# Kernel tuning notes

Hardware: AMD Instinct MI355X
Metric: run time of the kernel (lower is better)

The kernel has to match this reference:

```python
import jax, jax.numpy as jnp
import numpy as np

P = 8           # patch size
IMG = 256       # image size
C_IN = 64       # indim
HEADS = 32
DIM = P * P * C_IN          # 4096
SCALE = (DIM / HEADS) ** -0.5  # uses dim/heads = 128, as in the torch code
EPS = 1e-5


def unfold(x):
    # x: [B, C, H, W] -> [B, N, C*P*P]  (torch Unfold channel order: c, ki, kj)
    B, C, H, W = x.shape
    x = x.reshape(B, C, H // P, P, W // P, P)
    x = x.transpose(0, 1, 3, 5, 2, 4)           # [B, C, P, P, H/P, W/P]
    x = x.reshape(B, C * P * P, (H // P) * (W // P))
    return x.transpose(0, 2, 1)                  # b n c


def fold(x):
    # x: [B, C*P*P, N] -> [B, C, IMG, IMG]  (non-overlapping: exact inverse)
    B, Cpp, N = x.shape
    C = Cpp // (P * P)
    hp = IMG // P
    x = x.reshape(B, C, P, P, hp, hp)
    x = x.transpose(0, 1, 4, 2, 5, 3)            # [B, C, H/P, P, W/P, P]
    return x.reshape(B, C, IMG, IMG)


def layernorm(x, g, b):
    mu = jnp.mean(x, axis=-1, keepdims=True)
    var = jnp.mean(jnp.square(x - mu), axis=-1, keepdims=True)
    return (x - mu) * jax.lax.rsqrt(var + EPS) * g + b


def heads_split(x):
    # b n (g c) -> b g n c
    B, N, GC = x.shape
    return x.reshape(B, N, HEADS, GC // HEADS).transpose(0, 2, 1, 3)


def setup_inputs() -> dict:
    key = jax.random.key(0)
    ks = jax.random.split(key, 16)
    d = DIM
    def lin(k, din, dout):
        return jax.random.normal(k, (din, dout), jnp.float32) * (din ** -0.5)
    return {
        "pan": jax.random.normal(ks[0], (2, C_IN, IMG, IMG), jnp.float32),
        "ms": jax.random.normal(ks[1], (2, C_IN, IMG, IMG), jnp.float32),
        "g_q": jnp.ones((2 * d,), jnp.float32), "b_q": jnp.zeros((2 * d,), jnp.float32),
        "g_kp": jnp.ones((d,), jnp.float32), "b_kp": jnp.zeros((d,), jnp.float32),
        "g_vp": jnp.ones((d,), jnp.float32), "b_vp": jnp.zeros((d,), jnp.float32),
        "g_km": jnp.ones((d,), jnp.float32), "b_km": jnp.zeros((d,), jnp.float32),
        "g_vm": jnp.ones((d,), jnp.float32), "b_vm": jnp.zeros((d,), jnp.float32),
        "w_q": lin(ks[2], 2 * d, d // 4),
        "w_kp": lin(ks[3], d, d // 4),
        "w_vp": lin(ks[4], d, d),
        "w_km": lin(ks[5], d, d // 4),
        "w_vm": lin(ks[6], d, d),
    }


def _forward(pan, ms, g_q, b_q, g_kp, b_kp, g_vp, b_vp, g_km, b_km, g_vm, b_vm,
             w_q, w_kp, w_vp, w_km, w_vm):
    u_q = unfold(jnp.concatenate([pan, ms], axis=1))      # [B, N, 2*DIM]
    u_p = unfold(pan)                                     # [B, N, DIM]
    u_m = unfold(ms)                                      # [B, N, DIM]

    q = heads_split(layernorm(u_q, g_q, b_q) @ w_q)       # [B, G, N, 32]
    k_pan = heads_split(layernorm(u_p, g_kp, b_kp) @ w_kp)
    v_pan = heads_split(layernorm(u_p, g_vp, b_vp) @ w_vp)  # [B, G, N, 128]
    k_ms = heads_split(layernorm(u_m, g_km, b_km) @ w_km)
    v_ms = heads_split(layernorm(u_m, g_vm, b_vm) @ w_vm)

    def attend(k, v):
        logits = jnp.einsum('bgnc,bgmc->bgnm', q, k) * SCALE
        a = jax.nn.softmax(logits, axis=-1)
        o = jnp.einsum('bgnm,bgmc->bgnc', a, v)           # [B, G, N, 128]
        B, G, N, c = o.shape
        o = o.transpose(0, 2, 1, 3).reshape(B, N, G * c)  # b n (g c)
        return fold(o.transpose(0, 2, 1))                 # [B, C_IN, IMG, IMG]

    out_pan = attend(k_pan, v_pan) + pan
    out_ms = attend(k_ms, v_ms) + ms
    return jnp.concatenate([out_pan, out_ms], axis=1)


def reference(pan, ms, g_q, b_q, g_kp, b_kp, g_vp, b_vp, g_km, b_km, g_vm, b_vm,
              w_q, w_kp, w_vp, w_km, w_vm):
    return _forward(pan, ms, g_q, b_q, g_kp, b_kp, g_vp, b_vp, g_km, b_km,
                    g_vm, b_vm, w_q, w_kp, w_vp, w_km, w_vm)
```

## Files before the change

### kernel.cpp

```cpp
#include <hip/hip_runtime.h>
#include <hip/hip_bf16.h>

typedef __attribute__((ext_vector_type(8))) __bf16 bf16x8;
typedef __attribute__((ext_vector_type(8))) short s16x8;
typedef __attribute__((ext_vector_type(4))) float f32x4;

#define DEVI __device__ __forceinline__

DEVI f32x4 mfma16(bf16x8 a, bf16x8 b, f32x4 c) {
  return __builtin_amdgcn_mfma_f32_16x16x32_bf16((s16x8)a, (s16x8)b, c, 0, 0, 0);
}

constexpr float SCALE = 0.08838834764831845f;

constexpr size_t MB = 1024ull * 1024ull;
constexpr size_t OFF_WQT  = 0;
constexpr size_t OFF_WKPT = 16 * MB;
constexpr size_t OFF_WKMT = 24 * MB;
constexpr size_t OFF_LNQ  = 32 * MB;
constexpr size_t OFF_WVPT = 0;
constexpr size_t OFF_WVMT = 32 * MB;
constexpr size_t OFF_LNP  = 64 * MB;
constexpr size_t OFF_LNM  = 80 * MB;
constexpr size_t OFF_Q    = 96 * MB;
constexpr size_t OFF_KP   = 100 * MB;
constexpr size_t OFF_KM   = 104 * MB;
constexpr size_t OFF_VPT  = 108 * MB;
constexpr size_t OFF_VMT  = 124 * MB;
constexpr size_t OFF_BQ   = 140 * MB;
constexpr size_t OFF_BKP  = OFF_BQ  + 1024 * 4;
constexpr size_t OFF_BKM  = OFF_BKP + 1024 * 4;
constexpr size_t OFF_BVP  = OFF_BKM + 1024 * 4;
constexpr size_t OFF_BVM  = OFF_BVP + 4096 * 4;
constexpr int    N_BIAS_F = 3 * 1024 + 2 * 4096;

DEVI void async16(void* lds, const void* g) {
  __builtin_amdgcn_global_load_lds(
      (const __attribute__((address_space(1))) void*)g,
      (__attribute__((address_space(3))) void*)lds, 16, 0, 0);
}

__global__ void zero_kernel(float* p, int n) {
  int i = blockIdx.x * 256 + threadIdx.x;
  if (i < n) p[i] = 0.f;
}

__global__ __launch_bounds__(256) void wconv_kernel(
    const float* __restrict__ W, const float* __restrict__ gam,
    const float* __restrict__ bet, __bf16* __restrict__ wT,
    float* __restrict__ biasOut, int K, int N) {
  __shared__ float tile[64][65];
  const int n0 = blockIdx.x * 64, k0 = blockIdx.y * 64;
  const int t = threadIdx.x;
  const int nl = t & 63, kb = t >> 6;
  float pb = 0.f;
#pragma unroll
  for (int i = 0; i < 16; ++i) {
    const int kl = kb * 16 + i;
    const int k = k0 + kl;
    const float w = W[(long)k * N + n0 + nl];
    tile[kl][nl] = w * gam[k];
    pb += bet[k] * w;
  }
  atomicAdd(biasOut + n0 + nl, pb);
  __syncthreads();
  const int klw = t & 63;
#pragma unroll
  for (int i = 0; i < 16; ++i) {
    const int nloc = kb * 16 + i;
    wT[(long)(n0 + nloc) * K + k0 + klw] = (__bf16)tile[klw][nloc];
  }
}

__global__ __launch_bounds__(256) void ln_kernel(
    const float* __restrict__ pan, const float* __restrict__ ms,
    __bf16* __restrict__ lnq, __bf16* __restrict__ lnp, __bf16* __restrict__ lnm) {
  const int bid = blockIdx.x;
  const int b = bid >> 10, n = bid & 1023;
  const int ph = n >> 5, pw = n & 31;
  const int t = threadIdx.x;
  const int c = t >> 2, kp2 = t & 3;

  const long base = ((long)(b * 64 + c) << 16) + (long)(ph * 8) * 256 + pw * 8;
  float rp[16], rm[16];
#pragma unroll
  for (int kk = 0; kk < 2; ++kk) {
    const int ki = kp2 * 2 + kk;
    const f32x4* p0 = (const f32x4*)(pan + base + ki * 256);
    const f32x4* m0 = (const f32x4*)(ms + base + ki * 256);
    f32x4 pa = p0[0], pb = p0[1], ma = m0[0], mb = m0[1];
#pragma unroll
    for (int j = 0; j < 4; ++j) {
      rp[kk * 8 + j] = pa[j];
      rp[kk * 8 + 4 + j] = pb[j];
      rm[kk * 8 + j] = ma[j];
      rm[kk * 8 + 4 + j] = mb[j];
    }
  }
  float sp = 0, sp2 = 0, smm = 0, sm2 = 0;
#pragma unroll
  for (int j = 0; j < 16; ++j) {
    sp += rp[j]; sp2 += rp[j] * rp[j];
    smm += rm[j]; sm2 += rm[j] * rm[j];
  }
#pragma unroll
  for (int msk = 1; msk < 64; msk <<= 1) {
    sp += __shfl_xor(sp, msk);
    sp2 += __shfl_xor(sp2, msk);
    smm += __shfl_xor(smm, msk);
    sm2 += __shfl_xor(sm2, msk);
  }
  __shared__ float red[4][4];
  const int wid = t >> 6;
  if ((t & 63) == 0) { red[wid][0] = sp; red[wid][1] = sp2; red[wid][2] = smm; red[wid][3] = sm2; }
  __syncthreads();
  sp = red[0][0] + red[1][0] + red[2][0] + red[3][0];
  sp2 = red[0][1] + red[1][1] + red[2][1] + red[3][1];
  smm = red[0][2] + red[1][2] + red[2][2] + red[3][2];
  sm2 = red[0][3] + red[1][3] + red[2][3] + red[3][3];

  const float mu_p = sp * (1.f / 4096.f);
  const float rs_p = rsqrtf(sp2 * (1.f / 4096.f) - mu_p * mu_p + 1e-5f);
  const float mu_m = smm * (1.f / 4096.f);
  const float rs_m = rsqrtf(sm2 * (1.f / 4096.f) - mu_m * mu_m + 1e-5f);
  const float mu_q = (sp + smm) * (1.f / 8192.f);
  const float rs_q = rsqrtf((sp2 + sm2) * (1.f / 8192.f) - mu_q * mu_q + 1e-5f);

  const long row = bid;
  const int f0 = t * 16;
  bf16x8 v0, v1;
#pragma unroll
  for (int j = 0; j < 8; ++j) { v0[j] = (__bf16)((rp[j] - mu_p) * rs_p); v1[j] = (__bf16)((rp[8 + j] - mu_p) * rs_p); }
  *(bf16x8*)(lnp + row * 4096 + f0) = v0;
  *(bf16x8*)(lnp + row * 4096 + f0 + 8) = v1;
#pragma unroll
  for (int j = 0; j < 8; ++j) { v0[j] = (__bf16)((rm[j] - mu_m) * rs_m); v1[j] = (__bf16)((rm[8 + j] - mu_m) * rs_m); }
  *(bf16x8*)(lnm + row * 4096 + f0) = v0;
  *(bf16x8*)(lnm + row * 4096 + f0 + 8) = v1;
#pragma unroll
  for (int j = 0; j < 8; ++j) { v0[j] = (__bf16)((rp[j] - mu_q) * rs_q); v1[j] = (__bf16)((rp[8 + j] - mu_q) * rs_q); }
  *(bf16x8*)(lnq + row * 8192 + f0) = v0;
  *(bf16x8*)(lnq + row * 8192 + f0 + 8) = v1;
#pragma unroll
  for (int j = 0; j < 8; ++j) { v0[j] = (__bf16)((rm[j] - mu_q) * rs_q); v1[j] = (__bf16)((rm[8 + j] - mu_q) * rs_q); }
  *(bf16x8*)(lnq + row * 8192 + 4096 + f0) = v0;
  *(bf16x8*)(lnq + row * 8192 + 4096 + f0 + 8) = v1;
}

struct G3 {
  const __bf16 *X0, *X1, *X2, *Y0, *Y1, *Y2;
  __bf16 *O0, *O1, *O2;
  const float *bX0, *bX1, *bX2, *bY0, *bY1, *bY2;
  int K0, K1, K2, M2;
};

__global__ __launch_bounds__(256, 2) void gemm_batch(G3 g) {
  const int z = blockIdx.z;
  const __bf16* X = z == 0 ? g.X0 : (z == 1 ? g.X1 : g.X2);
  const __bf16* Y = z == 0 ? g.Y0 : (z == 1 ? g.Y1 : g.Y2);
  __bf16* out = z == 0 ? g.O0 : (z == 1 ? g.O1 : g.O2);
  const float* biasX = z == 0 ? g.bX0 : (z == 1 ? g.bX1 : g.bX2);
  const float* biasY = z == 0 ? g.bY0 : (z == 1 ? g.bY1 : g.bY2);
  const int K = z == 0 ? g.K0 : (z == 1 ? g.K1 : g.K2);
  const int M2 = g.M2;

  __shared__ __bf16 xt[128 * 32];
  __shared__ __bf16 yt[128 * 32];
  const int t = threadIdx.x;
  const int lane = t & 63, wid = t >> 6;
  const int wr = wid >> 1, wc = wid & 1;
  const int l15 = lane & 15, l4 = lane >> 4;
  const long x0 = (long)blockIdx.x * 128;
  const long y0 = (long)blockIdx.y * 128;

  f32x4 acc[4][4] = {};

  for (int kk = 0; kk < K; kk += 32) {
    __syncthreads();
#pragma unroll
    for (int i = 0; i < 2; ++i) {
      const int chunk = i * 256 + t;
      const int r = chunk >> 2, q = chunk & 3;
      async16((char*)xt + (i * 256 + wid * 64) * 16, X + (x0 + r) * K + kk + q * 8);
      async16((char*)yt + (i * 256 + wid * 64) * 16, Y + (y0 + r) * K + kk + q * 8);
    }
    __syncthreads();
    bf16x8 a[4], bb[4];
#pragma unroll
    for (int mi = 0; mi < 4; ++mi)
      a[mi] = *(const bf16x8*)(xt + (wr * 64 + mi * 16 + l15) * 32 + l4 * 8);
#pragma unroll
    for (int ni = 0; ni < 4; ++ni)
      bb[ni] = *(const bf16x8*)(yt + (wc * 64 + ni * 16 + l15) * 32 + l4 * 8);
#pragma unroll
    for (int mi = 0; mi < 4; ++mi)
#pragma unroll
      for (int ni = 0; ni < 4; ++ni)
        acc[mi][ni] = mfma16(a[mi], bb[ni], acc[mi][ni]);
  }

#pragma unroll
  for (int mi = 0; mi < 4; ++mi) {
#pragma unroll
    for (int r = 0; r < 4; ++r) {
      const long row = x0 + wr * 64 + mi * 16 + l4 * 4 + r;
      const float bx = biasX ? biasX[row] : 0.f;
#pragma unroll
      for (int ni = 0; ni < 4; ++ni) {
        const long col = y0 + wc * 64 + ni * 16 + l15;
        const float by = biasY ? biasY[col] : 0.f;
        out[row * M2 + col] = (__bf16)(acc[mi][ni][r] + bx + by);
      }
    }
  }
}

__global__ __launch_bounds__(256, 2) void attn_kernel(
    const __bf16* __restrict__ Qm, const __bf16* __restrict__ Kpm,
    const __bf16* __restrict__ Kmm, const __bf16* __restrict__ VpT,
    const __bf16* __restrict__ VmT, const float* __restrict__ pan,
    const float* __restrict__ ms, float* __restrict__ out) {
  __shared__ __bf16 ktile[128 * 32];
  __shared__ __bf16 vtile[128 * 128];
  __shared__ __bf16 ptile[4][32 * 128];

  const int bid = blockIdx.x;
  const int qt = bid & 7, g = (bid >> 3) & 31, tt = (bid >> 8) & 1, b = bid >> 9;
  const __bf16* Kmat = tt ? Kmm : Kpm;
  const __bf16* VT = tt ? VmT : VpT;
  const float* res = tt ? ms : pan;

  const int t = threadIdx.x, lane = t & 63, wid = t >> 6;
  const int l15 = lane & 15, l4 = lane >> 4;

  bf16x8 qf[2];
#pragma unroll
  for (int mi = 0; mi < 2; ++mi) {
    const long row = (long)b * 1024 + qt * 128 + wid * 32 + mi * 16 + l15;
    qf[mi] = *(const bf16x8*)(Qm + row * 1024 + g * 32 + l4 * 8);
  }

  f32x4 acc[2][8] = {};
  float mrun[2][4], lrun[2][4];
#pragma unroll
  for (int mi = 0; mi < 2; ++mi)
#pragma unroll
    for (int r = 0; r < 4; ++r) { mrun[mi][r] = -1e30f; lrun[mi][r] = 0.f; }

  for (int kt = 0; kt < 8; ++kt) {
    __syncthreads();
#pragma unroll
    for (int i = 0; i < 2; ++i) {
      const int chunk = i * 256 + t;
      const int key = chunk >> 2, slot = chunk & 3;
      const int q = slot ^ ((key >> 1) & 3);
      async16((char*)ktile + (i * 256 + wid * 64) * 16,
              Kmat + (long)(b * 1024 + kt * 128 + key) * 1024 + g * 32 + q * 8);
    }
#pragma unroll
    for (int i = 0; i < 8; ++i) {
      const int chunk = i * 256 + t;
      const int d = chunk >> 4, slot = chunk & 15;
      const int c16 = slot ^ (d & 15);
      async16((char*)vtile + (i * 256 + wid * 64) * 16,
              VT + (long)(g * 128 + d) * 2048 + b * 1024 + kt * 128 + c16 * 8);
    }
    __syncthreads();

    f32x4 s[2][8];
#pragma unroll
    for (int ni = 0; ni < 8; ++ni) {
      const int key = ni * 16 + l15;
      const int slot = l4 ^ ((key >> 1) & 3);
      const bf16x8 kf = *(const bf16x8*)(ktile + key * 32 + slot * 8);
      f32x4 zz = {0.f, 0.f, 0.f, 0.f};
      s[0][ni] = mfma16(qf[0], kf, zz);
      s[1][ni] = mfma16(qf[1], kf, zz);
    }

#pragma unroll
    for (int mi = 0; mi < 2; ++mi) {
#pragma unroll
      for (int r = 0; r < 4; ++r) {
        float tmax = -1e30f;
#pragma unroll
        for (int ni = 0; ni < 8; ++ni) tmax = fmaxf(tmax, s[mi][ni][r]);
        tmax *= SCALE;
#pragma unroll
        for (int msk = 1; msk < 16; msk <<= 1) tmax = fmaxf(tmax, __shfl_xor(tmax, msk));
        const float mnew = fmaxf(mrun[mi][r], tmax);
        const float alpha = __expf(mrun[mi][r] - mnew);
        mrun[mi][r] = mnew;
        float tsum = 0.f;
#pragma unroll
        for (int ni = 0; ni < 8; ++ni) {
          const float p = __expf(s[mi][ni][r] * SCALE - mnew);
          s[mi][ni][r] = p;
          tsum += p;
        }
#pragma unroll
        for (int msk = 1; msk < 16; msk <<= 1) tsum += __shfl_xor(tsum, msk);
        lrun[mi][r] = lrun[mi][r] * alpha + tsum;
#pragma unroll
        for (int ni = 0; ni < 8; ++ni) acc[mi][ni][r] *= alpha;
      }
    }

#pragma unroll
    for (int mi = 0; mi < 2; ++mi)
#pragma unroll
      for (int ni = 0; ni < 8; ++ni)
#pragma unroll
        for (int r = 0; r < 4; ++r) {
          const int q = mi * 16 + l4 * 4 + r;
          const int key = ni * 16 + l15;
          const int off = q * 256 + (((key >> 3) ^ (q & 15)) * 16) + (key & 7) * 2;
          *(__bf16*)((char*)ptile[wid] + off) = (__bf16)s[mi][ni][r];
        }
    __syncthreads();

#pragma unroll
    for (int ks = 0; ks < 4; ++ks) {
      bf16x8 pa[2];
#pragma unroll
      for (int mi = 0; mi < 2; ++mi) {
        const int q = mi * 16 + l15;
        const int slot = (ks * 4 + l4) ^ (q & 15);
        pa[mi] = *(const bf16x8*)((char*)ptile[wid] + q * 256 + slot * 16);
      }
#pragma unroll
      for (int ni = 0; ni < 8; ++ni) {
        const int d = ni * 16 + l15;
        const int slot = (ks * 4 + l4) ^ (d & 15);
        const bf16x8 vf = *(const bf16x8*)((char*)vtile + d * 256 + slot * 16);
        acc[0][ni] = mfma16(pa[0], vf, acc[0][ni]);
        acc[1][ni] = mfma16(pa[1], vf, acc[1][ni]);
      }
    }
  }

#pragma unroll
  for (int mi = 0; mi < 2; ++mi) {
#pragma unroll
    for (int r = 0; r < 4; ++r) {
      const float inv = 1.f / lrun[mi][r];
      const int n = qt * 128 + wid * 32 + mi * 16 + l4 * 4 + r;
      const int ph = n >> 5, pw = n & 31;
#pragma unroll
      for (int ni = 0; ni < 8; ++ni) {
        const int d = ni * 16 + l15;
        const int ch = 2 * g + (d >> 6);
        const int pix = (ph * 8 + ((d >> 3) & 7)) * 256 + pw * 8 + (d & 7);
        const long ridx = (long)(b * 64 + ch) * 65536 + pix;
        const long oidx = (long)(b * 128 + tt * 64 + ch) * 65536 + pix;
        out[oidx] = acc[mi][ni][r] * inv + res[ridx];
      }
    }
  }
}

extern "C" void kernel_launch(void* const* d_in, const int* in_sizes, int n_in,
                              void* d_out, int out_size, void* d_ws, size_t ws_size,
                              hipStream_t stream) {
  const float* pan = (const float*)d_in[0];
  const float* ms = (const float*)d_in[1];
  const float* g_q = (const float*)d_in[2];
  const float* b_q = (const float*)d_in[3];
  const float* g_kp = (const float*)d_in[4];
  const float* b_kp = (const float*)d_in[5];
  const float* g_vp = (const float*)d_in[6];
  const float* b_vp = (const float*)d_in[7];
  const float* g_km = (const float*)d_in[8];
  const float* b_km = (const float*)d_in[9];
  const float* g_vm = (const float*)d_in[10];
  const float* b_vm = (const float*)d_in[11];
  const float* w_q = (const float*)d_in[12];
  const float* w_kp = (const float*)d_in[13];
  const float* w_vp = (const float*)d_in[14];
  const float* w_km = (const float*)d_in[15];
  const float* w_vm = (const float*)d_in[16];

  char* ws = (char*)d_ws;
  __bf16* wqT = (__bf16*)(ws + OFF_WQT);
  __bf16* wkpT = (__bf16*)(ws + OFF_WKPT);
  __bf16* wkmT = (__bf16*)(ws + OFF_WKMT);
  __bf16* lnq = (__bf16*)(ws + OFF_LNQ);
  __bf16* wvpT = (__bf16*)(ws + OFF_WVPT);
  __bf16* wvmT = (__bf16*)(ws + OFF_WVMT);
  __bf16* lnp = (__bf16*)(ws + OFF_LNP);
  __bf16* lnm = (__bf16*)(ws + OFF_LNM);
  __bf16* Qm = (__bf16*)(ws + OFF_Q);
  __bf16* Kpm = (__bf16*)(ws + OFF_KP);
  __bf16* Kmm = (__bf16*)(ws + OFF_KM);
  __bf16* VpT = (__bf16*)(ws + OFF_VPT);
  __bf16* VmT = (__bf16*)(ws + OFF_VMT);
  float* bq = (float*)(ws + OFF_BQ);
  float* bkp = (float*)(ws + OFF_BKP);
  float* bkm = (float*)(ws + OFF_BKM);
  float* bvp = (float*)(ws + OFF_BVP);
  float* bvm = (float*)(ws + OFF_BVM);

  const dim3 blk(256);

  zero_kernel<<<(N_BIAS_F + 255) / 256, blk, 0, stream>>>(bq, N_BIAS_F);

  wconv_kernel<<<dim3(16, 128), blk, 0, stream>>>(w_q, g_q, b_q, wqT, bq, 8192, 1024);
  wconv_kernel<<<dim3(16, 64), blk, 0, stream>>>(w_kp, g_kp, b_kp, wkpT, bkp, 4096, 1024);
  wconv_kernel<<<dim3(16, 64), blk, 0, stream>>>(w_km, g_km, b_km, wkmT, bkm, 4096, 1024);

  ln_kernel<<<2048, blk, 0, stream>>>(pan, ms, lnq, lnp, lnm);

  {
    G3 g;
    g.X0 = lnq; g.X1 = lnp; g.X2 = lnm;
    g.Y0 = wqT; g.Y1 = wkpT; g.Y2 = wkmT;
    g.O0 = Qm; g.O1 = Kpm; g.O2 = Kmm;
    g.bX0 = nullptr; g.bX1 = nullptr; g.bX2 = nullptr;
    g.bY0 = bq; g.bY1 = bkp; g.bY2 = bkm;
    g.K0 = 8192; g.K1 = 4096; g.K2 = 4096; g.M2 = 1024;
    gemm_batch<<<dim3(16, 8, 3), blk, 0, stream>>>(g);
  }

  wconv_kernel<<<dim3(64, 64), blk, 0, stream>>>(w_vp, g_vp, b_vp, wvpT, bvp, 4096, 4096);
  wconv_kernel<<<dim3(64, 64), blk, 0, stream>>>(w_vm, g_vm, b_vm, wvmT, bvm, 4096, 4096);

  {
    G3 g;
    g.X0 = wvpT; g.X1 = wvmT; g.X2 = wvmT;
    g.Y0 = lnp; g.Y1 = lnm; g.Y2 = lnm;
    g.O0 = VpT; g.O1 = VmT; g.O2 = VmT;
    g.bX0 = bvp; g.bX1 = bvm; g.bX2 = bvm;
    g.bY0 = nullptr; g.bY1 = nullptr; g.bY2 = nullptr;
    g.K0 = 4096; g.K1 = 4096; g.K2 = 4096; g.M2 = 2048;
    gemm_batch<<<dim3(32, 16, 2), blk, 0, stream>>>(g);
  }

  attn_kernel<<<1024, blk, 0, stream>>>(Qm, Kpm, Kmm, VpT, VmT, pan, ms, (float*)d_out);
}
```

Baseline: 826.4 us.

## Halve attention key tiles for higher occupancy and swizzle GEMM block order

The attention kernel now processes keys in 64-key tiles instead of 128, which cuts shared memory per block. It raises the launch-bounds occupancy target from 2 to 4 blocks per CU and reorders block IDs so each query tile is the outer index over batch, type and head. The batched GEMM remaps its 2D block index with a stride-8 interleave to change L2 and XCD locality of tile scheduling. The trade-off is twice as many softmax rescale steps and barriers per block, plus tighter register limits that may cause spills.

```diff
diff --git a/kernel.cpp b/kernel.cpp
--- a/kernel.cpp
+++ b/kernel.cpp
@@ -164,14 +164,19 @@
   const int K = z == 0 ? g.K0 : (z == 1 ? g.K1 : g.K2);
   const int M2 = g.M2;
 
+  int lh = blockIdx.x + gridDim.x * blockIdx.y;
+  const int per = (gridDim.x * gridDim.y) >> 3;
+  lh = (lh & 7) * per + (lh >> 3);
+  const int bx = lh % gridDim.x, by = lh / gridDim.x;
+
   __shared__ __bf16 xt[128 * 32];
   __shared__ __bf16 yt[128 * 32];
   const int t = threadIdx.x;
   const int lane = t & 63, wid = t >> 6;
   const int wr = wid >> 1, wc = wid & 1;
   const int l15 = lane & 15, l4 = lane >> 4;
-  const long x0 = (long)blockIdx.x * 128;
-  const long y0 = (long)blockIdx.y * 128;
+  const long x0 = (long)bx * 128;
+  const long y0 = (long)by * 128;
 
   f32x4 acc[4][4] = {};
 
@@ -204,28 +209,29 @@
 #pragma unroll
     for (int r = 0; r < 4; ++r) {
       const long row = x0 + wr * 64 + mi * 16 + l4 * 4 + r;
-      const float bx = biasX ? biasX[row] : 0.f;
+      const float bx_ = biasX ? biasX[row] : 0.f;
 #pragma unroll
       for (int ni = 0; ni < 4; ++ni) {
         const long col = y0 + wc * 64 + ni * 16 + l15;
-        const float by = biasY ? biasY[col] : 0.f;
-        out[row * M2 + col] = (__bf16)(acc[mi][ni][r] + bx + by);
+        const float by_ = biasY ? biasY[col] : 0.f;
+        out[row * M2 + col] = (__bf16)(acc[mi][ni][r] + bx_ + by_);
       }
     }
   }
 }
 
-__global__ __launch_bounds__(256, 2) void attn_kernel(
+__global__ __launch_bounds__(256, 4) void attn_kernel(
     const __bf16* __restrict__ Qm, const __bf16* __restrict__ Kpm,
     const __bf16* __restrict__ Kmm, const __bf16* __restrict__ VpT,
     const __bf16* __restrict__ VmT, const float* __restrict__ pan,
     const float* __restrict__ ms, float* __restrict__ out) {
-  __shared__ __bf16 ktile[128 * 32];
-  __shared__ __bf16 vtile[128 * 128];
-  __shared__ __bf16 ptile[4][32 * 128];
+  __shared__ __bf16 ktile[64 * 32];
+  __shared__ __bf16 vtile[128 * 64];
+  __shared__ __bf16 ptile[4][32 * 64];
 
   const int bid = blockIdx.x;
-  const int qt = bid & 7, g = (bid >> 3) & 31, tt = (bid >> 8) & 1, b = bid >> 9;
+  const int qt = bid >> 7, gid = bid & 127;
+  const int b = gid >> 6, tt = (gid >> 5) & 1, g = gid & 31;
   const __bf16* Kmat = tt ? Kmm : Kpm;
   const __bf16* VT = tt ? VmT : VpT;
   const float* res = tt ? ms : pan;
@@ -247,29 +253,27 @@
 #pragma unroll
     for (int r = 0; r < 4; ++r) { mrun[mi][r] = -1e30f; lrun[mi][r] = 0.f; }
 
-  for (int kt = 0; kt < 8; ++kt) {
+  for (int kt = 0; kt < 16; ++kt) {
     __syncthreads();
-#pragma unroll
-    for (int i = 0; i < 2; ++i) {
+    {
+      const int key = t >> 2, slot = t & 3;
+      const int q = slot ^ ((key >> 1) & 3);
+      async16((char*)ktile + t * 16,
+              Kmat + (long)(b * 1024 + kt * 64 + key) * 1024 + g * 32 + q * 8);
+    }
+#pragma unroll
+    for (int i = 0; i < 4; ++i) {
       const int chunk = i * 256 + t;
-      const int key = chunk >> 2, slot = chunk & 3;
-      const int q = slot ^ ((key >> 1) & 3);
-      async16((char*)ktile + (i * 256 + wid * 64) * 16,
-              Kmat + (long)(b * 1024 + kt * 128 + key) * 1024 + g * 32 + q * 8);
-    }
-#pragma unroll
-    for (int i = 0; i < 8; ++i) {
-      const int chunk = i * 256 + t;
-      const int d = chunk >> 4, slot = chunk & 15;
-      const int c16 = slot ^ (d & 15);
-      async16((char*)vtile + (i * 256 + wid * 64) * 16,
-              VT + (long)(g * 128 + d) * 2048 + b * 1024 + kt * 128 + c16 * 8);
+      const int d = chunk >> 3, slot = chunk & 7;
+      const int c8 = slot ^ (d & 7);
+      async16((char*)vtile + chunk * 16,
+              VT + (long)(g * 128 + d) * 2048 + b * 1024 + kt * 64 + c8 * 8);
     }
     __syncthreads();
 
-    f32x4 s[2][8];
-#pragma unroll
-    for (int ni = 0; ni < 8; ++ni) {
+    f32x4 s[2][4];
+#pragma unroll
+    for (int ni = 0; ni < 4; ++ni) {
       const int key = ni * 16 + l15;
       const int slot = l4 ^ ((key >> 1) & 3);
       const bf16x8 kf = *(const bf16x8*)(ktile + key * 32 + slot * 8);
@@ -284,7 +288,7 @@
       for (int r = 0; r < 4; ++r) {
         float tmax = -1e30f;
 #pragma unroll
-        for (int ni = 0; ni < 8; ++ni) tmax = fmaxf(tmax, s[mi][ni][r]);
+        for (int ni = 0; ni < 4; ++ni) tmax = fmaxf(tmax, s[mi][ni][r]);
         tmax *= SCALE;
 #pragma unroll
         for (int msk = 1; msk < 16; msk <<= 1) tmax = fmaxf(tmax, __shfl_xor(tmax, msk));
@@ -293,7 +297,7 @@
         mrun[mi][r] = mnew;
         float tsum = 0.f;
 #pragma unroll
-        for (int ni = 0; ni < 8; ++ni) {
+        for (int ni = 0; ni < 4; ++ni) {
           const float p = __expf(s[mi][ni][r] * SCALE - mnew);
           s[mi][ni][r] = p;
           tsum += p;
@@ -302,37 +306,39 @@
         for (int msk = 1; msk < 16; msk <<= 1) tsum += __shfl_xor(tsum, msk);
         lrun[mi][r] = lrun[mi][r] * alpha + tsum;
 #pragma unroll
-        for (int ni = 0; ni < 8; ++ni) acc[mi][ni][r] *= alpha;
+        for (int ni = 0; ni < 4; ++ni) acc[mi][ni][r] *= alpha;
+#pragma unroll
+        for (int ni = 4; ni < 8; ++ni) acc[mi][ni][r] *= alpha;
       }
     }
 
 #pragma unroll
     for (int mi = 0; mi < 2; ++mi)
 #pragma unroll
-      for (int ni = 0; ni < 8; ++ni)
+      for (int ni = 0; ni < 4; ++ni)
 #pragma unroll
         for (int r = 0; r < 4; ++r) {
           const int q = mi * 16 + l4 * 4 + r;
           const int key = ni * 16 + l15;
-          const int off = q * 256 + (((key >> 3) ^ (q & 15)) * 16) + (key & 7) * 2;
+          const int off = q * 128 + (((key >> 3) ^ (q & 7)) * 16) + (key & 7) * 2;
           *(__bf16*)((char*)ptile[wid] + off) = (__bf16)s[mi][ni][r];
         }
     __syncthreads();
 
 #pragma unroll
-    for (int ks = 0; ks < 4; ++ks) {
+    for (int ks = 0; ks < 2; ++ks) {
       bf16x8 pa[2];
 #pragma unroll
       for (int mi = 0; mi < 2; ++mi) {
         const int q = mi * 16 + l15;
-        const int slot = (ks * 4 + l4) ^ (q & 15);
-        pa[mi] = *(const bf16x8*)((char*)ptile[wid] + q * 256 + slot * 16);
+        const int slot = (ks * 4 + l4) ^ (q & 7);
+        pa[mi] = *(const bf16x8*)((char*)ptile[wid] + q * 128 + slot * 16);
       }
 #pragma unroll
       for (int ni = 0; ni < 8; ++ni) {
         const int d = ni * 16 + l15;
-        const int slot = (ks * 4 + l4) ^ (d & 15);
-        const bf16x8 vf = *(const bf16x8*)((char*)vtile + d * 256 + slot * 16);
+        const int slot = (ks * 4 + l4) ^ (d & 7);
+        const bf16x8 vf = *(const bf16x8*)((char*)vtile + d * 128 + slot * 16);
         acc[0][ni] = mfma16(pa[0], vf, acc[0][ni]);
         acc[1][ni] = mfma16(pa[1], vf, acc[1][ni]);
       }
```

After: 1.021 ms. 1.24x slower.

## Keep softmax probabilities in registers via transposed MFMA and vectorize epilogue stores

Applied to the files above, without the earlier changes.

The attention kernel computes S^T by swapping MFMA operands and permuting the key rows as they load into LDS, so the probability tile already has the register layout needed as the B operand of the PV MFMA. This removes the per-warp LDS round trip for P and the extra __syncthreads. Softmax statistics become one value per row per lane, reduced across lanes with two shuffles. LDS use falls, so launch bounds go to 3 blocks per CU. The epilogue stages each output tile through LDS and writes it with 16-byte vectorized residual loads and stores. The GEMM also swizzles its block indices for better cache locality. Risks include register pressure at the higher occupancy and subtle layout errors in the key permutation.

```diff
diff --git a/kernel.cpp b/kernel.cpp
--- a/kernel.cpp
+++ b/kernel.cpp
@@ -2,6 +2,7 @@
 #include <hip/hip_bf16.h>
 
 typedef __attribute__((ext_vector_type(8))) __bf16 bf16x8;
+typedef __attribute__((ext_vector_type(4))) __bf16 bf16x4;
 typedef __attribute__((ext_vector_type(8))) short s16x8;
 typedef __attribute__((ext_vector_type(4))) float f32x4;
 
@@ -164,14 +165,19 @@
   const int K = z == 0 ? g.K0 : (z == 1 ? g.K1 : g.K2);
   const int M2 = g.M2;
 
+  int lh = blockIdx.x + gridDim.x * blockIdx.y;
+  const int per = (gridDim.x * gridDim.y) >> 3;
+  lh = (lh & 7) * per + (lh >> 3);
+  const int bx = lh % gridDim.x, by = lh / gridDim.x;
+
   __shared__ __bf16 xt[128 * 32];
   __shared__ __bf16 yt[128 * 32];
   const int t = threadIdx.x;
   const int lane = t & 63, wid = t >> 6;
   const int wr = wid >> 1, wc = wid & 1;
   const int l15 = lane & 15, l4 = lane >> 4;
-  const long x0 = (long)blockIdx.x * 128;
-  const long y0 = (long)blockIdx.y * 128;
+  const long x0 = (long)bx * 128;
+  const long y0 = (long)by * 128;
 
   f32x4 acc[4][4] = {};
 
@@ -204,25 +210,25 @@
 #pragma unroll
     for (int r = 0; r < 4; ++r) {
       const long row = x0 + wr * 64 + mi * 16 + l4 * 4 + r;
-      const float bx = biasX ? biasX[row] : 0.f;
+      const float bx_ = biasX ? biasX[row] : 0.f;
 #pragma unroll
       for (int ni = 0; ni < 4; ++ni) {
         const long col = y0 + wc * 64 + ni * 16 + l15;
-        const float by = biasY ? biasY[col] : 0.f;
-        out[row * M2 + col] = (__bf16)(acc[mi][ni][r] + bx + by);
+        const float by_ = biasY ? biasY[col] : 0.f;
+        out[row * M2 + col] = (__bf16)(acc[mi][ni][r] + bx_ + by_);
       }
     }
   }
 }
 
-__global__ __launch_bounds__(256, 2) void attn_kernel(
+__global__ __launch_bounds__(256, 3) void attn_kernel(
     const __bf16* __restrict__ Qm, const __bf16* __restrict__ Kpm,
     const __bf16* __restrict__ Kmm, const __bf16* __restrict__ VpT,
     const __bf16* __restrict__ VmT, const float* __restrict__ pan,
     const float* __restrict__ ms, float* __restrict__ out) {
-  __shared__ __bf16 ktile[128 * 32];
-  __shared__ __bf16 vtile[128 * 128];
-  __shared__ __bf16 ptile[4][32 * 128];
+  __shared__ char smem[40960];
+  __bf16* ktile = (__bf16*)smem;
+  __bf16* vtile = (__bf16*)(smem + 8192);
 
   const int bid = blockIdx.x;
   const int qt = bid & 7, g = (bid >> 3) & 31, tt = (bid >> 8) & 1, b = bid >> 9;
@@ -241,21 +247,18 @@
   }
 
   f32x4 acc[2][8] = {};
-  float mrun[2][4], lrun[2][4];
-#pragma unroll
-  for (int mi = 0; mi < 2; ++mi)
-#pragma unroll
-    for (int r = 0; r < 4; ++r) { mrun[mi][r] = -1e30f; lrun[mi][r] = 0.f; }
+  float mrun[2] = {-1e30f, -1e30f}, lrun[2] = {0.f, 0.f};
 
   for (int kt = 0; kt < 8; ++kt) {
     __syncthreads();
 #pragma unroll
     for (int i = 0; i < 2; ++i) {
       const int chunk = i * 256 + t;
-      const int key = chunk >> 2, slot = chunk & 3;
-      const int q = slot ^ ((key >> 1) & 3);
+      const int rho = chunk >> 2, slot = chunk & 3;
+      const int cq = slot ^ ((rho >> 1) & 3);
+      const int keyg = 32 * (rho >> 5) + 8 * ((rho >> 2) & 3) + 4 * ((rho >> 4) & 1) + (rho & 3);
       async16((char*)ktile + (i * 256 + wid * 64) * 16,
-              Kmat + (long)(b * 1024 + kt * 128 + key) * 1024 + g * 32 + q * 8);
+              Kmat + (long)(b * 1024 + kt * 128 + keyg) * 1024 + g * 32 + cq * 8);
     }
 #pragma unroll
     for (int i = 0; i < 8; ++i) {
@@ -267,95 +270,95 @@
     }
     __syncthreads();
 
-    f32x4 s[2][8];
-#pragma unroll
-    for (int ni = 0; ni < 8; ++ni) {
-      const int key = ni * 16 + l15;
-      const int slot = l4 ^ ((key >> 1) & 3);
-      const bf16x8 kf = *(const bf16x8*)(ktile + key * 32 + slot * 8);
-      f32x4 zz = {0.f, 0.f, 0.f, 0.f};
-      s[0][ni] = mfma16(qf[0], kf, zz);
-      s[1][ni] = mfma16(qf[1], kf, zz);
-    }
-
+    bf16x4 pk[2][8];
 #pragma unroll
     for (int mi = 0; mi < 2; ++mi) {
-#pragma unroll
-      for (int r = 0; r < 4; ++r) {
-        float tmax = -1e30f;
-#pragma unroll
-        for (int ni = 0; ni < 8; ++ni) tmax = fmaxf(tmax, s[mi][ni][r]);
-        tmax *= SCALE;
-#pragma unroll
-        for (int msk = 1; msk < 16; msk <<= 1) tmax = fmaxf(tmax, __shfl_xor(tmax, msk));
-        const float mnew = fmaxf(mrun[mi][r], tmax);
-        const float alpha = __expf(mrun[mi][r] - mnew);
-        mrun[mi][r] = mnew;
-        float tsum = 0.f;
-#pragma unroll
-        for (int ni = 0; ni < 8; ++ni) {
-          const float p = __expf(s[mi][ni][r] * SCALE - mnew);
-          s[mi][ni][r] = p;
+      f32x4 s[8];
+#pragma unroll
+      for (int ni = 0; ni < 8; ++ni) {
+        const int pos = ni * 16 + l15;
+        const int slot = l4 ^ ((pos >> 1) & 3);
+        const bf16x8 kf = *(const bf16x8*)(ktile + pos * 32 + slot * 8);
+        f32x4 zz = {0.f, 0.f, 0.f, 0.f};
+        s[ni] = mfma16(kf, qf[mi], zz);
+      }
+      float tmax = -1e30f;
+#pragma unroll
+      for (int ni = 0; ni < 8; ++ni)
+#pragma unroll
+        for (int r = 0; r < 4; ++r) tmax = fmaxf(tmax, s[ni][r]);
+      tmax *= SCALE;
+      tmax = fmaxf(tmax, __shfl_xor(tmax, 16));
+      tmax = fmaxf(tmax, __shfl_xor(tmax, 32));
+      const float mnew = fmaxf(mrun[mi], tmax);
+      const float alpha = __expf(mrun[mi] - mnew);
+      mrun[mi] = mnew;
+      float tsum = 0.f;
+#pragma unroll
+      for (int ni = 0; ni < 8; ++ni)
+#pragma unroll
+        for (int r = 0; r < 4; ++r) {
+          const float p = __expf(s[ni][r] * SCALE - mnew);
+          pk[mi][ni][r] = (__bf16)p;
           tsum += p;
         }
-#pragma unroll
-        for (int msk = 1; msk < 16; msk <<= 1) tsum += __shfl_xor(tsum, msk);
-        lrun[mi][r] = lrun[mi][r] * alpha + tsum;
-#pragma unroll
-        for (int ni = 0; ni < 8; ++ni) acc[mi][ni][r] *= alpha;
-      }
-    }
-
-#pragma unroll
-    for (int mi = 0; mi < 2; ++mi)
-#pragma unroll
-      for (int ni = 0; ni < 8; ++ni)
-#pragma unroll
-        for (int r = 0; r < 4; ++r) {
-          const int q = mi * 16 + l4 * 4 + r;
-          const int key = ni * 16 + l15;
-          const int off = q * 256 + (((key >> 3) ^ (q & 15)) * 16) + (key & 7) * 2;
-          *(__bf16*)((char*)ptile[wid] + off) = (__bf16)s[mi][ni][r];
-        }
-    __syncthreads();
+      tsum += __shfl_xor(tsum, 16);
+      tsum += __shfl_xor(tsum, 32);
+      lrun[mi] = lrun[mi] * alpha + tsum;
+#pragma unroll
+      for (int ni = 0; ni < 8; ++ni) acc[mi][ni] *= alpha;
+    }
 
 #pragma unroll
     for (int ks = 0; ks < 4; ++ks) {
-      bf16x8 pa[2];
-#pragma unroll
-      for (int mi = 0; mi < 2; ++mi) {
-        const int q = mi * 16 + l15;
-        const int slot = (ks * 4 + l4) ^ (q & 15);
-        pa[mi] = *(const bf16x8*)((char*)ptile[wid] + q * 256 + slot * 16);
+      bf16x8 pf0, pf1;
+#pragma unroll
+      for (int j = 0; j < 4; ++j) {
+        pf0[j] = pk[0][2 * ks][j];
+        pf0[4 + j] = pk[0][2 * ks + 1][j];
+        pf1[j] = pk[1][2 * ks][j];
+        pf1[4 + j] = pk[1][2 * ks + 1][j];
       }
 #pragma unroll
       for (int ni = 0; ni < 8; ++ni) {
         const int d = ni * 16 + l15;
         const int slot = (ks * 4 + l4) ^ (d & 15);
-        const bf16x8 vf = *(const bf16x8*)((char*)vtile + d * 256 + slot * 16);
-        acc[0][ni] = mfma16(pa[0], vf, acc[0][ni]);
-        acc[1][ni] = mfma16(pa[1], vf, acc[1][ni]);
+        const bf16x8 vf = *(const bf16x8*)(vtile + d * 128 + slot * 8);
+        acc[0][ni] = mfma16(vf, pf0, acc[0][ni]);
+        acc[1][ni] = mfma16(vf, pf1, acc[1][ni]);
       }
     }
   }
 
+  __syncthreads();
+  float* ldsT = (float*)(smem + wid * 8448);
 #pragma unroll
   for (int mi = 0; mi < 2; ++mi) {
-#pragma unroll
-    for (int r = 0; r < 4; ++r) {
-      const float inv = 1.f / lrun[mi][r];
-      const int n = qt * 128 + wid * 32 + mi * 16 + l4 * 4 + r;
-      const int ph = n >> 5, pw = n & 31;
-#pragma unroll
-      for (int ni = 0; ni < 8; ++ni) {
-        const int d = ni * 16 + l15;
-        const int ch = 2 * g + (d >> 6);
-        const int pix = (ph * 8 + ((d >> 3) & 7)) * 256 + pw * 8 + (d & 7);
-        const long ridx = (long)(b * 64 + ch) * 65536 + pix;
-        const long oidx = (long)(b * 128 + tt * 64 + ch) * 65536 + pix;
-        out[oidx] = acc[mi][ni][r] * inv + res[ridx];
-      }
-    }
+    const float inv = 1.f / lrun[mi];
+#pragma unroll
+    for (int ni = 0; ni < 8; ++ni) {
+      f32x4 v = acc[mi][ni];
+      v.x *= inv; v.y *= inv; v.z *= inv; v.w *= inv;
+      *(f32x4*)(ldsT + l15 * 132 + ni * 16 + l4 * 4) = v;
+    }
+    asm volatile("s_waitcnt lgkmcnt(0)" ::: "memory");
+    __builtin_amdgcn_sched_barrier(0);
+    const int n = qt * 128 + wid * 32 + mi * 16 + l15;
+    const int ph = n >> 5, pw = n & 31;
+#pragma unroll
+    for (int j = 0; j < 8; ++j) {
+      const int d0 = (l4 * 8 + j) * 4;
+      const f32x4 v = *(const f32x4*)(ldsT + l15 * 132 + d0);
+      const int ch = 2 * g + (d0 >> 6);
+      const int pix = (ph * 8 + ((d0 >> 3) & 7)) * 256 + pw * 8 + (d0 & 7);
+      const long ridx = (long)(b * 64 + ch) * 65536 + pix;
+      const long oidx = (long)(b * 128 + tt * 64 + ch) * 65536 + pix;
+      const f32x4 rv = *(const f32x4*)(res + ridx);
+      f32x4 o;
+      o.x = v.x + rv.x; o.y = v.y + rv.y; o.z = v.z + rv.z; o.w = v.w + rv.w;
+      *(f32x4*)(out + oidx) = o;
+    }
+    asm volatile("s_waitcnt lgkmcnt(0)" ::: "memory");
   }
 }
 
```

Result: no change. 831.4 us (+0.6%).
